# Optimization experiments

Hardware: AMD Instinct MI355X
Metric: run time of the kernel (lower is better)

Reference implementation:

```python
import jax, jax.numpy as jnp
import numpy as np
from jax import lax

V, E, H, K = 50257, 256, 256, 3
T, B, S = 1024, 32, 1024


def setup_inputs() -> dict:
    key = jax.random.key(0)
    ks = jax.random.split(key, 10)
    inp = {
        "source": jax.random.randint(ks[0], (T, B), 0, V),
        "target": jax.random.randint(ks[1], (T, B), 0, V),
        "enc_attn": jax.random.normal(ks[2], (B, S, H), jnp.float32),
        "source_seq_out": jax.random.normal(ks[3], (B, S, 2 * H), jnp.float32),
        "emb": jax.random.normal(ks[4], (V, E), jnp.float32) * 0.02,
        "affine_w": jax.random.normal(ks[5], (2 * H, E), jnp.float32) * 0.02,
        "affine_b": jnp.zeros((2 * H,), jnp.float32),
        "conv_w": jax.random.normal(ks[6], (2 * H, 1, K, 2 * H), jnp.float32) * 0.02,
        "conv_b": jnp.zeros((2 * H,), jnp.float32),
        "map_w": jax.random.normal(ks[7], (2 * H, H), jnp.float32) * 0.02,
        "map_b": jnp.zeros((2 * H,), jnp.float32),
    }
    return inp


def reference(source, target, enc_attn, source_seq_out, emb, affine_w, affine_b,
              conv_w, conv_b, map_w, map_b):
    # source is unused by the original forward (kept for signature fidelity)
    x = emb[target]                                   # [T, B, E]
    x = x @ affine_w.T + affine_b                     # [T, B, 2H]
    x = jnp.transpose(x, (1, 0, 2))                   # [B, T, 2H]  (.t() swaps dims 0,1)
    x = x[:, None, :, :]                              # [B, 1, T, 2H]
    # conv2d: out_ch=2H, kernel=(K, 2H), padding=(K-1, 0) -> [B, 2H, T+K-1, 1]
    y = lax.conv_general_dilated(
        x, conv_w, window_strides=(1, 1),
        padding=((K - 1, K - 1), (0, 0)),
        dimension_numbers=("NCHW", "OIHW", "NCHW"))
    y = y + conv_b[None, :, None, None]
    y = y[:, :, : y.shape[2] - K, :]                  # narrow -> length L = T - 1 (faithful)
    y = jax.nn.relu(y)
    y = jnp.transpose(y[..., 0], (0, 2, 1))           # [B, L, 2H]
    A, Bg = y[..., :H], y[..., H:]                    # GLU split
    dec_attn = A * jax.nn.softmax(Bg, axis=-1)        # [B, L, H]
    dec_attn2 = dec_attn @ map_w.T + map_b            # [B, L, 2H]
    scores = jnp.einsum("blh,bsh->bls", dec_attn, enc_attn)   # [B, L, S]
    attn = jax.nn.softmax(scores, axis=-1)
    attns = jnp.einsum("bls,bsd->bld", attn, source_seq_out)  # [B, L, 2H]
    return dec_attn2 + attns
```

## Files before the change

kernel.cpp:

```cpp
#include <hip/hip_runtime.h>
#include <stdint.h>


typedef __bf16 bf16x8_t __attribute__((ext_vector_type(8)));
typedef float  f32x4_t  __attribute__((ext_vector_type(4)));

#define DEV __device__ __forceinline__

DEV unsigned short f2bf(float f) {
  union { float f; unsigned u; } v; v.f = f;
  unsigned r = v.u + 0x7fffu + ((v.u >> 16) & 1u);
  return (unsigned short)(r >> 16);
}
DEV float bf2f(unsigned short u) {
  union { unsigned u; float f; } v; v.u = ((unsigned)u) << 16;
  return v.f;
}

DEV void gload_lds16(const void* g, void* l) {
  __builtin_amdgcn_global_load_lds((const __attribute__((address_space(1))) void*)g,
                                   (__attribute__((address_space(3))) void*)l, 16, 0, 0);
}

__global__ void zero_k(unsigned short* p) { p[threadIdx.x] = 0; }

__global__ __launch_bounds__(256) void zero_rows_k(float* p) {
  int i = (blockIdx.x * 256 + threadIdx.x) * 4;
  *(float4*)(p + i) = make_float4(0.f, 0.f, 0.f, 0.f);
}

__global__ __launch_bounds__(256) void cvt_bf16_k(const float* __restrict__ src,
                                                  unsigned short* __restrict__ dst,
                                                  int n) {
  int i = (blockIdx.x * 256 + threadIdx.x) * 4;
  if (i >= n) return;
  float4 v = *(const float4*)(src + i);
  ushort4 o;
  o.x = f2bf(v.x); o.y = f2bf(v.y); o.z = f2bf(v.z); o.w = f2bf(v.w);
  *(ushort4*)(dst + i) = o;
}

__global__ __launch_bounds__(256) void cvt_transpose_v_k(const float* __restrict__ src,
                                                         unsigned short* __restrict__ dst) {
  __shared__ float tile[32][33];
  int b = blockIdx.z, s0 = blockIdx.x * 32, d0 = blockIdx.y * 32;
  int tx = threadIdx.x & 31, ty = threadIdx.x >> 5;
  const float* p = src + ((size_t)b * 1024 + s0) * 512 + d0;
  for (int r = ty; r < 32; r += 8) tile[r][tx] = p[(size_t)r * 512 + tx];
  __syncthreads();
  unsigned short* q = dst + ((size_t)b * 512 + d0) * 1024 + s0;
  for (int r = ty; r < 32; r += 8) q[(size_t)r * 1024 + tx] = f2bf(tile[tx][r]);
}

__global__ __launch_bounds__(256) void embed_affine_k(const int* __restrict__ tgt,
                                                      const float* __restrict__ emb,
                                                      const unsigned short* __restrict__ awb,
                                                      const float* __restrict__ ab,
                                                      unsigned short* __restrict__ X) {
  constexpr int AP = 264;
  __shared__ unsigned short xs[32 * AP];
  const int r0 = blockIdx.x * 32;
  const int tid = threadIdx.x;
  for (int idx = tid; idx < 32 * 64; idx += 256) {
    int r = idx >> 6, c4 = (idx & 63) * 4;
    int row = tgt[r0 + r];
    float4 v = *(const float4*)&emb[(size_t)row * 256 + c4];
    ushort4 o;
    o.x = f2bf(v.x); o.y = f2bf(v.y); o.z = f2bf(v.z); o.w = f2bf(v.w);
    *(ushort4*)&xs[r * AP + c4] = o;
  }
  __syncthreads();
  const int lane = tid & 63, w = tid >> 6, q = lane >> 4, ln = lane & 15;
  f32x4_t acc[2][8];
#pragma unroll
  for (int mt = 0; mt < 2; ++mt)
#pragma unroll
    for (int nt = 0; nt < 8; ++nt) acc[mt][nt] = (f32x4_t){0.f, 0.f, 0.f, 0.f};
  for (int kk = 0; kk < 256; kk += 32) {
    bf16x8_t a[2], bb[8];
#pragma unroll
    for (int mt = 0; mt < 2; ++mt)
      a[mt] = *(const bf16x8_t*)(xs + (mt * 16 + ln) * AP + kk + q * 8);
#pragma unroll
    for (int nt = 0; nt < 8; ++nt) {
      int n = ((w * 8 + nt) << 4) + ln;
      bb[nt] = *(const bf16x8_t*)(awb + ((size_t)n << 8) + kk + q * 8);
    }
#pragma unroll
    for (int mt = 0; mt < 2; ++mt)
#pragma unroll
      for (int nt = 0; nt < 8; ++nt)
        acc[mt][nt] = __builtin_amdgcn_mfma_f32_16x16x32_bf16(a[mt], bb[nt], acc[mt][nt], 0, 0, 0);
  }
#pragma unroll
  for (int nt = 0; nt < 8; ++nt) {
    const int o = ((w * 8 + nt) << 4) + ln;
    const float bias = ab[o];
#pragma unroll
    for (int mt = 0; mt < 2; ++mt)
#pragma unroll
      for (int r = 0; r < 4; ++r) {
        int rid = r0 + mt * 16 + q * 4 + r;
        int t = rid >> 5, b = rid & 31;
        X[(((size_t)(b * 1024 + t)) << 9) + o] = f2bf(acc[mt][nt][r] + bias);
      }
  }
}

DEV void cstage(unsigned short* AsB, unsigned short* BsB,
                const unsigned short* __restrict__ X,
                const unsigned short* __restrict__ Wc,
                const unsigned short* __restrict__ zbuf,
                int b, int l0, int n0, int t, int w, int srow, int scolg) {
  const int kk = t << 5;
  const int i  = kk >> 9;
  const int c0 = kk & 511;
  {
    const int lr = l0 + srow + i - 2;
    const unsigned short* sp = (lr < 0)
        ? (zbuf + scolg * 8)
        : (X + (((size_t)(b * 1024 + lr)) << 9) + c0 + scolg * 8);
    gload_lds16(sp, AsB + w * 512);
  }
  {
    const int lr = l0 + 64 + srow + i - 2;
    gload_lds16(X + (((size_t)(b * 1024 + lr)) << 9) + c0 + scolg * 8,
                AsB + 2048 + w * 512);
  }
  gload_lds16(Wc + (size_t)(n0 + srow) * 1536 + kk + scolg * 8, BsB + w * 512);
  gload_lds16(Wc + (size_t)(n0 + 64 + srow) * 1536 + kk + scolg * 8,
              BsB + 2048 + w * 512);
}

__global__ __launch_bounds__(256) void conv_gemm_k(const unsigned short* __restrict__ X,
                                                   const unsigned short* __restrict__ Wc,
                                                   const float* __restrict__ cb,
                                                   const unsigned short* __restrict__ zbuf,
                                                   unsigned short* __restrict__ Y) {
  __shared__ unsigned short As[2][4096];
  __shared__ unsigned short Bs[2][4096];
  const int bid = blockIdx.x;
  const int mtile = bid >> 2;
  const int b  = mtile >> 3;
  const int l0 = (mtile & 7) << 7;
  const int n0 = (bid & 3) << 7;
  const int tid = threadIdx.x;
  const int w = tid >> 6, lane = tid & 63, q = lane >> 4, ln = lane & 15;
  const int wr = w >> 1, wc = w & 1;
  const int srow = tid >> 2, scolg = tid & 3;

  f32x4_t acc[4][4];
#pragma unroll
  for (int mt = 0; mt < 4; ++mt)
#pragma unroll
    for (int nt = 0; nt < 4; ++nt) acc[mt][nt] = (f32x4_t){0.f, 0.f, 0.f, 0.f};

  cstage(As[0], Bs[0], X, Wc, zbuf, b, l0, n0, 0, w, srow, scolg);
  __syncthreads();

  for (int t = 0; t < 48; ++t) {
    const int cur = t & 1;
    if (t < 47)
      cstage(As[cur ^ 1], Bs[cur ^ 1], X, Wc, zbuf, b, l0, n0, t + 1, w, srow, scolg);
    const unsigned short* Ab = As[cur];
    const unsigned short* Bb = Bs[cur];
    bf16x8_t af[4], bf[4];
#pragma unroll
    for (int x = 0; x < 4; ++x) {
      af[x] = *(const bf16x8_t*)(Ab + (wr * 64 + x * 16 + ln) * 32 + q * 8);
      bf[x] = *(const bf16x8_t*)(Bb + (wc * 64 + x * 16 + ln) * 32 + q * 8);
    }
#pragma unroll
    for (int mt = 0; mt < 4; ++mt)
#pragma unroll
      for (int nt = 0; nt < 4; ++nt)
        acc[mt][nt] = __builtin_amdgcn_mfma_f32_16x16x32_bf16(af[mt], bf[nt], acc[mt][nt], 0, 0, 0);
    __syncthreads();
  }

#pragma unroll
  for (int nt = 0; nt < 4; ++nt) {
    const int o = n0 + wc * 64 + nt * 16 + ln;
    const float bias = cb[o];
#pragma unroll
    for (int mt = 0; mt < 4; ++mt)
#pragma unroll
      for (int r = 0; r < 4; ++r) {
        const int l = l0 + wr * 64 + mt * 16 + q * 4 + r;
        float v = acc[mt][nt][r] + bias;
        Y[(((size_t)b * 1024 + l) << 9) + o] = f2bf(v > 0.f ? v : 0.f);
      }
  }
}

__global__ __launch_bounds__(256) void glu_k(const unsigned short* __restrict__ Y,
                                             unsigned short* __restrict__ dec) {
  const int row = blockIdx.x * 4 + (threadIdx.x >> 6);
  const int lane = threadIdx.x & 63;
  const unsigned short* p = Y + ((size_t)row << 9);
  ushort4 av = *(const ushort4*)(p + lane * 4);
  ushort4 gv = *(const ushort4*)(p + 256 + lane * 4);
  float e0 = __expf(bf2f(gv.x)), e1 = __expf(bf2f(gv.y));
  float e2 = __expf(bf2f(gv.z)), e3 = __expf(bf2f(gv.w));
  float s = e0 + e1 + e2 + e3;
#pragma unroll
  for (int off = 32; off > 0; off >>= 1) s += __shfl_xor(s, off);
  float inv = 1.f / s;
  ushort4 o;
  o.x = f2bf(bf2f(av.x) * e0 * inv);
  o.y = f2bf(bf2f(av.y) * e1 * inv);
  o.z = f2bf(bf2f(av.z) * e2 * inv);
  o.w = f2bf(bf2f(av.w) * e3 * inv);
  *(ushort4*)(dec + ((size_t)row << 8) + lane * 4) = o;
}

DEV void gstage(unsigned short* AsB, unsigned short* BsB,
                const unsigned short* __restrict__ Arow,
                const unsigned short* __restrict__ Brow,
                int strideA, int strideB, int kk, int w, int srow, int scolg) {
  gload_lds16(Arow + (size_t)srow * strideA + kk + scolg * 8, AsB + w * 512);
  gload_lds16(Arow + (size_t)(64 + srow) * strideA + kk + scolg * 8,
              AsB + 2048 + w * 512);
  gload_lds16(Brow + (size_t)srow * strideB + kk + scolg * 8, BsB + w * 512);
  gload_lds16(Brow + (size_t)(64 + srow) * strideB + kk + scolg * 8,
              BsB + 2048 + w * 512);
}

__global__ __launch_bounds__(256) void attn_s_k(const unsigned short* __restrict__ dec,
                                                const unsigned short* __restrict__ enc,
                                                unsigned short* __restrict__ P,
                                                float* __restrict__ rows) {
  __shared__ unsigned short As[2][4096];
  __shared__ unsigned short Bs[2][4096];
  const int bid = blockIdx.x;
  const int wg = ((bid & 7) << 8) + (bid >> 3);
  const int ntile = wg & 7, mtile = wg >> 3;
  const int b = mtile >> 3;
  const int row0 = mtile << 7;
  const int s0 = ntile << 7;
  const int tid = threadIdx.x;
  const int w = tid >> 6, lane = tid & 63, q = lane >> 4, ln = lane & 15;
  const int wr = w >> 1, wc = w & 1;
  const int srow = tid >> 2, scolg = tid & 3;

  const unsigned short* Ab = dec + ((size_t)row0 << 8);
  const unsigned short* Bb = enc + ((size_t)b << 18) + ((size_t)s0 << 8);

  f32x4_t acc[4][4];
#pragma unroll
  for (int mt = 0; mt < 4; ++mt)
#pragma unroll
    for (int nt = 0; nt < 4; ++nt) acc[mt][nt] = (f32x4_t){0.f, 0.f, 0.f, 0.f};

  gstage(As[0], Bs[0], Ab, Bb, 256, 256, 0, w, srow, scolg);
  __syncthreads();

  for (int t = 0; t < 8; ++t) {
    const int cur = t & 1;
    if (t < 7)
      gstage(As[cur ^ 1], Bs[cur ^ 1], Ab, Bb, 256, 256, (t + 1) << 5, w, srow, scolg);
    const unsigned short* Ap = As[cur];
    const unsigned short* Bp = Bs[cur];
    bf16x8_t af[4], bf[4];
#pragma unroll
    for (int x = 0; x < 4; ++x) {
      af[x] = *(const bf16x8_t*)(Ap + (wr * 64 + x * 16 + ln) * 32 + q * 8);
      bf[x] = *(const bf16x8_t*)(Bp + (wc * 64 + x * 16 + ln) * 32 + q * 8);
    }
#pragma unroll
    for (int mt = 0; mt < 4; ++mt)
#pragma unroll
      for (int nt = 0; nt < 4; ++nt)
        acc[mt][nt] = __builtin_amdgcn_mfma_f32_16x16x32_bf16(af[mt], bf[nt], acc[mt][nt], 0, 0, 0);
    __syncthreads();
  }

  float rs[4][4];
#pragma unroll
  for (int mt = 0; mt < 4; ++mt)
#pragma unroll
    for (int r = 0; r < 4; ++r) rs[mt][r] = 0.f;
#pragma unroll
  for (int nt = 0; nt < 4; ++nt) {
    const int col = s0 + wc * 64 + nt * 16 + ln;
#pragma unroll
    for (int mt = 0; mt < 4; ++mt)
#pragma unroll
      for (int r = 0; r < 4; ++r) {
        const int row = row0 + wr * 64 + mt * 16 + q * 4 + r;
        float e = __expf(acc[mt][nt][r]);
        rs[mt][r] += e;
        P[((size_t)row << 10) + col] = f2bf(e);
      }
  }
#pragma unroll
  for (int mt = 0; mt < 4; ++mt)
#pragma unroll
    for (int r = 0; r < 4; ++r) {
      float v = rs[mt][r];
      v += __shfl_xor(v, 1); v += __shfl_xor(v, 2);
      v += __shfl_xor(v, 4); v += __shfl_xor(v, 8);
      if (ln == 0)
        atomicAdd(&rows[row0 + wr * 64 + mt * 16 + q * 4 + r], v);
    }
}

__global__ __launch_bounds__(256) void attn_pv_k(const unsigned short* __restrict__ P,
                                                 const unsigned short* __restrict__ vt,
                                                 const unsigned short* __restrict__ dec,
                                                 const unsigned short* __restrict__ mw,
                                                 const float* __restrict__ rows,
                                                 const float* __restrict__ mb,
                                                 float* __restrict__ out) {
  __shared__ unsigned short As[2][4096];
  __shared__ unsigned short Bs[2][4096];
  const int bid = blockIdx.x;
  const int wg = ((bid & 7) << 7) + (bid >> 3);
  const int ntile = wg & 3, mtile = wg >> 2;
  const int b = mtile >> 3;
  const int row0 = mtile << 7;
  const int d0 = ntile << 7;
  const int tid = threadIdx.x;
  const int w = tid >> 6, lane = tid & 63, q = lane >> 4, ln = lane & 15;
  const int wr = w >> 1, wc = w & 1;
  const int srow = tid >> 2, scolg = tid & 3;

  const unsigned short* A1 = P + ((size_t)row0 << 10);
  const unsigned short* B1 = vt + ((size_t)b << 19) + ((size_t)d0 << 10);
  const unsigned short* A2 = dec + ((size_t)row0 << 8);
  const unsigned short* B2 = mw + ((size_t)d0 << 8);

  float rinv[4][4];
#pragma unroll
  for (int mt = 0; mt < 4; ++mt)
#pragma unroll
    for (int r = 0; r < 4; ++r)
      rinv[mt][r] = 1.f / rows[row0 + wr * 64 + mt * 16 + q * 4 + r];

  f32x4_t acc[4][4];
#pragma unroll
  for (int mt = 0; mt < 4; ++mt)
#pragma unroll
    for (int nt = 0; nt < 4; ++nt) acc[mt][nt] = (f32x4_t){0.f, 0.f, 0.f, 0.f};

  gstage(As[0], Bs[0], A1, B1, 1024, 1024, 0, w, srow, scolg);
  __syncthreads();

  for (int t = 0; t < 40; ++t) {
    const int cur = t & 1;
    if (t < 39) {
      const int tn = t + 1;
      if (tn < 32)
        gstage(As[cur ^ 1], Bs[cur ^ 1], A1, B1, 1024, 1024, tn << 5, w, srow, scolg);
      else
        gstage(As[cur ^ 1], Bs[cur ^ 1], A2, B2, 256, 256, (tn - 32) << 5, w, srow, scolg);
    }
    const unsigned short* Ap = As[cur];
    const unsigned short* Bp = Bs[cur];
    bf16x8_t af[4], bf[4];
#pragma unroll
    for (int x = 0; x < 4; ++x) {
      af[x] = *(const bf16x8_t*)(Ap + (wr * 64 + x * 16 + ln) * 32 + q * 8);
      bf[x] = *(const bf16x8_t*)(Bp + (wc * 64 + x * 16 + ln) * 32 + q * 8);
    }
#pragma unroll
    for (int mt = 0; mt < 4; ++mt)
#pragma unroll
      for (int nt = 0; nt < 4; ++nt)
        acc[mt][nt] = __builtin_amdgcn_mfma_f32_16x16x32_bf16(af[mt], bf[nt], acc[mt][nt], 0, 0, 0);
    if (t == 31) {
#pragma unroll
      for (int mt = 0; mt < 4; ++mt)
#pragma unroll
        for (int nt = 0; nt < 4; ++nt)
#pragma unroll
          for (int r = 0; r < 4; ++r) acc[mt][nt][r] *= rinv[mt][r];
    }
    __syncthreads();
  }

#pragma unroll
  for (int nt = 0; nt < 4; ++nt) {
    const int d = d0 + wc * 64 + nt * 16 + ln;
    const float bias = mb[d];
#pragma unroll
    for (int mt = 0; mt < 4; ++mt)
#pragma unroll
      for (int r = 0; r < 4; ++r) {
        const int row = row0 + wr * 64 + mt * 16 + q * 4 + r;
        const int l = row & 1023;
        if (l < 1023)
          out[((size_t)b * 1023 + l) * 512 + d] = acc[mt][nt][r] + bias;
      }
  }
}

extern "C" void kernel_launch(void* const* d_in, const int* in_sizes, int n_in,
                              void* d_out, int out_size, void* d_ws, size_t ws_size,
                              hipStream_t stream) {
  const int*   target = (const int*)d_in[1];
  const float* enc    = (const float*)d_in[2];
  const float* src    = (const float*)d_in[3];
  const float* emb    = (const float*)d_in[4];
  const float* aw     = (const float*)d_in[5];
  const float* ab     = (const float*)d_in[6];
  const float* cw     = (const float*)d_in[7];
  const float* cb     = (const float*)d_in[8];
  const float* mw     = (const float*)d_in[9];
  const float* mb     = (const float*)d_in[10];
  float* out = (float*)d_out;
  char* ws = (char*)d_ws;

  unsigned short* Xbf  = (unsigned short*)(ws);
  unsigned short* Ybf  = (unsigned short*)(ws + 33554432);
  unsigned short* Pb   = (unsigned short*)(ws);
  unsigned short* dec  = (unsigned short*)(ws + 67108864);
  unsigned short* encb = (unsigned short*)(ws + 83886080);
  unsigned short* vtb  = (unsigned short*)(ws + 100663296);
  unsigned short* wcb  = (unsigned short*)(ws + 134217728);
  float*          rows = (float*)(ws + 134217728);
  unsigned short* mwb  = (unsigned short*)(ws + 135790592);
  unsigned short* awb  = (unsigned short*)(ws + 136052736);

  zero_k<<<1, 512, 0, stream>>>(dec);
  cvt_bf16_k<<<8192, 256, 0, stream>>>(enc, encb, 32 * 1024 * 256);
  cvt_bf16_k<<<768, 256, 0, stream>>>(cw, wcb, 512 * 1536);
  cvt_bf16_k<<<128, 256, 0, stream>>>(mw, mwb, 512 * 256);
  cvt_bf16_k<<<128, 256, 0, stream>>>(aw, awb, 512 * 256);
  cvt_transpose_v_k<<<dim3(32, 16, 32), 256, 0, stream>>>(src, vtb);
  embed_affine_k<<<1024, 256, 0, stream>>>(target, emb, awb, ab, Xbf);
  conv_gemm_k<<<1024, 256, 0, stream>>>(Xbf, wcb, cb, dec, Ybf);
  zero_rows_k<<<32, 256, 0, stream>>>(rows);
  glu_k<<<8192, 256, 0, stream>>>(Ybf, dec);
  attn_s_k<<<2048, 256, 0, stream>>>(dec, encb, Pb, rows);
  attn_pv_k<<<1024, 256, 0, stream>>>(Pb, vtb, dec, mwb, rows, mb, out);
}
```

Baseline: 452.5 us.

## Use 64-wide K tiles with XOR-swizzled LDS and vmcnt-based barriers in GEMMs

Doubles the K step of the conv, score and PV GEMM kernels from 32 to 64, halving the number of loop iterations and barriers. LDS tiles are stored with an XOR swizzle on 16-byte column groups to avoid bank conflicts on fragment reads. __syncthreads is replaced with explicit s_waitcnt vmcnt(8)/lgkmcnt(0) plus s_barrier, so the next stage's async global-to-LDS loads stay in flight while the current stage computes. The conv kernel's block-to-tile mapping is also reordered for locality. LDS use doubles, which may lower occupancy.

```diff
diff --git a/kernel.cpp b/kernel.cpp
--- a/kernel.cpp
+++ b/kernel.cpp
@@ -20,6 +20,47 @@
 DEV void gload_lds16(const void* g, void* l) {
   __builtin_amdgcn_global_load_lds((const __attribute__((address_space(1))) void*)g,
                                    (__attribute__((address_space(3))) void*)l, 16, 0, 0);
+}
+
+DEV void vm8_bar() {
+  asm volatile("s_waitcnt vmcnt(8)" ::: "memory");
+  __builtin_amdgcn_s_barrier();
+}
+DEV void vm0_bar() {
+  asm volatile("s_waitcnt vmcnt(0)" ::: "memory");
+  __builtin_amdgcn_s_barrier();
+}
+DEV void lgkm_bar() {
+  asm volatile("s_waitcnt lgkmcnt(0)" ::: "memory");
+  __builtin_amdgcn_s_barrier();
+}
+
+DEV void sstage64(unsigned short* AsB, unsigned short* BsB,
+                  const unsigned short* __restrict__ Arow,
+                  const unsigned short* __restrict__ Brow,
+                  int strideA, int strideB, int kk, int tid) {
+#pragma unroll
+  for (int g = 0; g < 4; ++g) {
+    const int gid = g * 256 + tid;
+    const int r = gid >> 3;
+    const int cs = (((gid & 7) ^ (r & 7)) << 3);
+    gload_lds16(Arow + (size_t)r * strideA + kk + cs, AsB + gid * 8);
+    gload_lds16(Brow + (size_t)r * strideB + kk + cs, BsB + gid * 8);
+  }
+}
+
+DEV void fragread(bf16x8_t (&af)[4], bf16x8_t (&bff)[4],
+                  const unsigned short* __restrict__ Ab,
+                  const unsigned short* __restrict__ Bb,
+                  int wr, int wc, int h, int q, int ln) {
+  const int G = (h << 2) + q;
+#pragma unroll
+  for (int x = 0; x < 4; ++x) {
+    const int ra = wr * 64 + x * 16 + ln;
+    const int rb = wc * 64 + x * 16 + ln;
+    af[x]  = *(const bf16x8_t*)(Ab + ra * 64 + ((G ^ (ra & 7)) << 3));
+    bff[x] = *(const bf16x8_t*)(Bb + rb * 64 + ((G ^ (rb & 7)) << 3));
+  }
 }
 
 __global__ void zero_k(unsigned short* p) { p[threadIdx.x] = 0; }
@@ -107,29 +148,24 @@
   }
 }
 
-DEV void cstage(unsigned short* AsB, unsigned short* BsB,
-                const unsigned short* __restrict__ X,
-                const unsigned short* __restrict__ Wc,
-                const unsigned short* __restrict__ zbuf,
-                int b, int l0, int n0, int t, int w, int srow, int scolg) {
-  const int kk = t << 5;
-  const int i  = kk >> 9;
-  const int c0 = kk & 511;
-  {
-    const int lr = l0 + srow + i - 2;
+DEV void cstage64(unsigned short* AsB, unsigned short* BsB,
+                  const unsigned short* __restrict__ X,
+                  const unsigned short* __restrict__ Wc,
+                  const unsigned short* __restrict__ zbuf,
+                  int b, int l0, int n0, int t, int tid) {
+  const int i = t >> 3, c0 = (t & 7) << 6;
+#pragma unroll
+  for (int g = 0; g < 4; ++g) {
+    const int gid = g * 256 + tid;
+    const int r = gid >> 3;
+    const int cs = (((gid & 7) ^ (r & 7)) << 3);
+    const int lr = l0 + r + i - 2;
     const unsigned short* sp = (lr < 0)
-        ? (zbuf + scolg * 8)
-        : (X + (((size_t)(b * 1024 + lr)) << 9) + c0 + scolg * 8);
-    gload_lds16(sp, AsB + w * 512);
-  }
-  {
-    const int lr = l0 + 64 + srow + i - 2;
-    gload_lds16(X + (((size_t)(b * 1024 + lr)) << 9) + c0 + scolg * 8,
-                AsB + 2048 + w * 512);
-  }
-  gload_lds16(Wc + (size_t)(n0 + srow) * 1536 + kk + scolg * 8, BsB + w * 512);
-  gload_lds16(Wc + (size_t)(n0 + 64 + srow) * 1536 + kk + scolg * 8,
-              BsB + 2048 + w * 512);
+        ? (zbuf + cs)
+        : (X + (((size_t)(b * 1024 + lr)) << 9) + c0 + cs);
+    gload_lds16(sp, AsB + gid * 8);
+    gload_lds16(Wc + (size_t)(n0 + r) * 1536 + (t << 6) + cs, BsB + gid * 8);
+  }
 }
 
 __global__ __launch_bounds__(256) void conv_gemm_k(const unsigned short* __restrict__ X,
@@ -137,17 +173,17 @@
                                                    const float* __restrict__ cb,
                                                    const unsigned short* __restrict__ zbuf,
                                                    unsigned short* __restrict__ Y) {
-  __shared__ unsigned short As[2][4096];
-  __shared__ unsigned short Bs[2][4096];
+  __shared__ unsigned short As[2][8192];
+  __shared__ unsigned short Bs[2][8192];
   const int bid = blockIdx.x;
-  const int mtile = bid >> 2;
+  const int mtile = ((bid >> 5) << 3) | (bid & 7);
+  const int ntile = (bid >> 3) & 3;
   const int b  = mtile >> 3;
   const int l0 = (mtile & 7) << 7;
-  const int n0 = (bid & 3) << 7;
+  const int n0 = ntile << 7;
   const int tid = threadIdx.x;
   const int w = tid >> 6, lane = tid & 63, q = lane >> 4, ln = lane & 15;
   const int wr = w >> 1, wc = w & 1;
-  const int srow = tid >> 2, scolg = tid & 3;
 
   f32x4_t acc[4][4];
 #pragma unroll
@@ -155,27 +191,27 @@
 #pragma unroll
     for (int nt = 0; nt < 4; ++nt) acc[mt][nt] = (f32x4_t){0.f, 0.f, 0.f, 0.f};
 
-  cstage(As[0], Bs[0], X, Wc, zbuf, b, l0, n0, 0, w, srow, scolg);
-  __syncthreads();
-
-  for (int t = 0; t < 48; ++t) {
+  cstage64(As[0], Bs[0], X, Wc, zbuf, b, l0, n0, 0, tid);
+
+  for (int t = 0; t < 24; ++t) {
     const int cur = t & 1;
-    if (t < 47)
-      cstage(As[cur ^ 1], Bs[cur ^ 1], X, Wc, zbuf, b, l0, n0, t + 1, w, srow, scolg);
-    const unsigned short* Ab = As[cur];
-    const unsigned short* Bb = Bs[cur];
-    bf16x8_t af[4], bf[4];
-#pragma unroll
-    for (int x = 0; x < 4; ++x) {
-      af[x] = *(const bf16x8_t*)(Ab + (wr * 64 + x * 16 + ln) * 32 + q * 8);
-      bf[x] = *(const bf16x8_t*)(Bb + (wc * 64 + x * 16 + ln) * 32 + q * 8);
-    }
-#pragma unroll
-    for (int mt = 0; mt < 4; ++mt)
-#pragma unroll
-      for (int nt = 0; nt < 4; ++nt)
-        acc[mt][nt] = __builtin_amdgcn_mfma_f32_16x16x32_bf16(af[mt], bf[nt], acc[mt][nt], 0, 0, 0);
-    __syncthreads();
+    if (t < 23) {
+      cstage64(As[cur ^ 1], Bs[cur ^ 1], X, Wc, zbuf, b, l0, n0, t + 1, tid);
+      vm8_bar();
+    } else {
+      vm0_bar();
+    }
+#pragma unroll
+    for (int h = 0; h < 2; ++h) {
+      bf16x8_t af[4], bff[4];
+      fragread(af, bff, As[cur], Bs[cur], wr, wc, h, q, ln);
+#pragma unroll
+      for (int mt = 0; mt < 4; ++mt)
+#pragma unroll
+        for (int nt = 0; nt < 4; ++nt)
+          acc[mt][nt] = __builtin_amdgcn_mfma_f32_16x16x32_bf16(af[mt], bff[nt], acc[mt][nt], 0, 0, 0);
+    }
+    lgkm_bar();
   }
 
 #pragma unroll
@@ -214,24 +250,12 @@
   *(ushort4*)(dec + ((size_t)row << 8) + lane * 4) = o;
 }
 
-DEV void gstage(unsigned short* AsB, unsigned short* BsB,
-                const unsigned short* __restrict__ Arow,
-                const unsigned short* __restrict__ Brow,
-                int strideA, int strideB, int kk, int w, int srow, int scolg) {
-  gload_lds16(Arow + (size_t)srow * strideA + kk + scolg * 8, AsB + w * 512);
-  gload_lds16(Arow + (size_t)(64 + srow) * strideA + kk + scolg * 8,
-              AsB + 2048 + w * 512);
-  gload_lds16(Brow + (size_t)srow * strideB + kk + scolg * 8, BsB + w * 512);
-  gload_lds16(Brow + (size_t)(64 + srow) * strideB + kk + scolg * 8,
-              BsB + 2048 + w * 512);
-}
-
 __global__ __launch_bounds__(256) void attn_s_k(const unsigned short* __restrict__ dec,
                                                 const unsigned short* __restrict__ enc,
                                                 unsigned short* __restrict__ P,
                                                 float* __restrict__ rows) {
-  __shared__ unsigned short As[2][4096];
-  __shared__ unsigned short Bs[2][4096];
+  __shared__ unsigned short As[2][8192];
+  __shared__ unsigned short Bs[2][8192];
   const int bid = blockIdx.x;
   const int wg = ((bid & 7) << 8) + (bid >> 3);
   const int ntile = wg & 7, mtile = wg >> 3;
@@ -241,7 +265,6 @@
   const int tid = threadIdx.x;
   const int w = tid >> 6, lane = tid & 63, q = lane >> 4, ln = lane & 15;
   const int wr = w >> 1, wc = w & 1;
-  const int srow = tid >> 2, scolg = tid & 3;
 
   const unsigned short* Ab = dec + ((size_t)row0 << 8);
   const unsigned short* Bb = enc + ((size_t)b << 18) + ((size_t)s0 << 8);
@@ -252,27 +275,27 @@
 #pragma unroll
     for (int nt = 0; nt < 4; ++nt) acc[mt][nt] = (f32x4_t){0.f, 0.f, 0.f, 0.f};
 
-  gstage(As[0], Bs[0], Ab, Bb, 256, 256, 0, w, srow, scolg);
-  __syncthreads();
-
-  for (int t = 0; t < 8; ++t) {
+  sstage64(As[0], Bs[0], Ab, Bb, 256, 256, 0, tid);
+
+  for (int t = 0; t < 4; ++t) {
     const int cur = t & 1;
-    if (t < 7)
-      gstage(As[cur ^ 1], Bs[cur ^ 1], Ab, Bb, 256, 256, (t + 1) << 5, w, srow, scolg);
-    const unsigned short* Ap = As[cur];
-    const unsigned short* Bp = Bs[cur];
-    bf16x8_t af[4], bf[4];
-#pragma unroll
-    for (int x = 0; x < 4; ++x) {
-      af[x] = *(const bf16x8_t*)(Ap + (wr * 64 + x * 16 + ln) * 32 + q * 8);
-      bf[x] = *(const bf16x8_t*)(Bp + (wc * 64 + x * 16 + ln) * 32 + q * 8);
-    }
-#pragma unroll
-    for (int mt = 0; mt < 4; ++mt)
-#pragma unroll
-      for (int nt = 0; nt < 4; ++nt)
-        acc[mt][nt] = __builtin_amdgcn_mfma_f32_16x16x32_bf16(af[mt], bf[nt], acc[mt][nt], 0, 0, 0);
-    __syncthreads();
+    if (t < 3) {
+      sstage64(As[cur ^ 1], Bs[cur ^ 1], Ab, Bb, 256, 256, (t + 1) << 6, tid);
+      vm8_bar();
+    } else {
+      vm0_bar();
+    }
+#pragma unroll
+    for (int h = 0; h < 2; ++h) {
+      bf16x8_t af[4], bff[4];
+      fragread(af, bff, As[cur], Bs[cur], wr, wc, h, q, ln);
+#pragma unroll
+      for (int mt = 0; mt < 4; ++mt)
+#pragma unroll
+        for (int nt = 0; nt < 4; ++nt)
+          acc[mt][nt] = __builtin_amdgcn_mfma_f32_16x16x32_bf16(af[mt], bff[nt], acc[mt][nt], 0, 0, 0);
+    }
+    lgkm_bar();
   }
 
   float rs[4][4];
@@ -312,8 +335,8 @@
                                                  const float* __restrict__ rows,
                                                  const float* __restrict__ mb,
                                                  float* __restrict__ out) {
-  __shared__ unsigned short As[2][4096];
-  __shared__ unsigned short Bs[2][4096];
+  __shared__ unsigned short As[2][8192];
+  __shared__ unsigned short Bs[2][8192];
   const int bid = blockIdx.x;
   const int wg = ((bid & 7) << 7) + (bid >> 3);
   const int ntile = wg & 3, mtile = wg >> 2;
@@ -323,7 +346,6 @@
   const int tid = threadIdx.x;
   const int w = tid >> 6, lane = tid & 63, q = lane >> 4, ln = lane & 15;
   const int wr = w >> 1, wc = w & 1;
-  const int srow = tid >> 2, scolg = tid & 3;
 
   const unsigned short* A1 = P + ((size_t)row0 << 10);
   const unsigned short* B1 = vt + ((size_t)b << 19) + ((size_t)d0 << 10);
@@ -343,40 +365,39 @@
 #pragma unroll
     for (int nt = 0; nt < 4; ++nt) acc[mt][nt] = (f32x4_t){0.f, 0.f, 0.f, 0.f};
 
-  gstage(As[0], Bs[0], A1, B1, 1024, 1024, 0, w, srow, scolg);
-  __syncthreads();
-
-  for (int t = 0; t < 40; ++t) {
+  sstage64(As[0], Bs[0], A1, B1, 1024, 1024, 0, tid);
+
+  for (int t = 0; t < 20; ++t) {
     const int cur = t & 1;
-    if (t < 39) {
+    if (t < 19) {
       const int tn = t + 1;
-      if (tn < 32)
-        gstage(As[cur ^ 1], Bs[cur ^ 1], A1, B1, 1024, 1024, tn << 5, w, srow, scolg);
+      if (tn < 16)
+        sstage64(As[cur ^ 1], Bs[cur ^ 1], A1, B1, 1024, 1024, tn << 6, tid);
       else
-        gstage(As[cur ^ 1], Bs[cur ^ 1], A2, B2, 256, 256, (tn - 32) << 5, w, srow, scolg);
-    }
-    const unsigned short* Ap = As[cur];
-    const unsigned short* Bp = Bs[cur];
-    bf16x8_t af[4], bf[4];
-#pragma unroll
-    for (int x = 0; x < 4; ++x) {
-      af[x] = *(const bf16x8_t*)(Ap + (wr * 64 + x * 16 + ln) * 32 + q * 8);
-      bf[x] = *(const bf16x8_t*)(Bp + (wc * 64 + x * 16 + ln) * 32 + q * 8);
-    }
-#pragma unroll
-    for (int mt = 0; mt < 4; ++mt)
-#pragma unroll
-      for (int nt = 0; nt < 4; ++nt)
-        acc[mt][nt] = __builtin_amdgcn_mfma_f32_16x16x32_bf16(af[mt], bf[nt], acc[mt][nt], 0, 0, 0);
-    if (t == 31) {
+        sstage64(As[cur ^ 1], Bs[cur ^ 1], A2, B2, 256, 256, (tn - 16) << 6, tid);
+      vm8_bar();
+    } else {
+      vm0_bar();
+    }
+#pragma unroll
+    for (int h = 0; h < 2; ++h) {
+      bf16x8_t af[4], bff[4];
+      fragread(af, bff, As[cur], Bs[cur], wr, wc, h, q, ln);
 #pragma unroll
       for (int mt = 0; mt < 4; ++mt)
 #pragma unroll
         for (int nt = 0; nt < 4; ++nt)
+          acc[mt][nt] = __builtin_amdgcn_mfma_f32_16x16x32_bf16(af[mt], bff[nt], acc[mt][nt], 0, 0, 0);
+    }
+    if (t == 15) {
+#pragma unroll
+      for (int mt = 0; mt < 4; ++mt)
+#pragma unroll
+        for (int nt = 0; nt < 4; ++nt)
 #pragma unroll
           for (int r = 0; r < 4; ++r) acc[mt][nt][r] *= rinv[mt][r];
     }
-    __syncthreads();
+    lgkm_bar();
   }
 
 #pragma unroll
```

After: 440.6 us. 2.6% less time.
